# Performance work log

Measured on AMD Instinct MI355X. Metric: run time of the kernel, lower is better.

Reference implementation:

```python
import jax, jax.numpy as jnp
from jax import lax
import numpy as np

H = 64  # LSTM_HIDDEN_DIM
I = 3   # NUM_WEATHER_FEATURES


def _lstm_layer(x_seq, w_ih, w_hh, b_ih, b_hh):
    # x_seq: [B, T, in]; w_ih: [4H, in]; w_hh: [4H, H]; b_*: [4H]
    B = x_seq.shape[0]
    # Precompute input projections for all timesteps: [T, B, 4H]
    gx = jnp.einsum('bti,gi->tbg', x_seq, w_ih) + (b_ih + b_hh)
    h0 = jnp.zeros((B, H), dtype=x_seq.dtype)
    c0 = jnp.zeros((B, H), dtype=x_seq.dtype)

    def step(carry, g_t):
        h, c = carry
        gates = g_t + h @ w_hh.T  # [B, 4H]
        i, f, g, o = jnp.split(gates, 4, axis=-1)  # PyTorch gate order i,f,g,o
        i = jax.nn.sigmoid(i)
        f = jax.nn.sigmoid(f)
        g = jnp.tanh(g)
        o = jax.nn.sigmoid(o)
        c = f * c + i * g
        h = o * jnp.tanh(c)
        return (h, c), h

    (h_T, _), hs = lax.scan(step, (h0, c0), gx)
    # hs: [T, B, H] -> [B, T, H]
    return jnp.transpose(hs, (1, 0, 2)), h_T


def setup_inputs() -> dict:
    key = jax.random.key(0)
    ks = jax.random.split(key, 9)
    s = 1.0 / np.sqrt(H)  # PyTorch LSTM init scale
    x = jax.random.normal(ks[0], (4096, 365, I), dtype=jnp.float32)
    return {
        'x': x,
        'w_ih0': jax.random.uniform(ks[1], (4 * H, I), jnp.float32, -s, s),
        'w_hh0': jax.random.uniform(ks[2], (4 * H, H), jnp.float32, -s, s),
        'b_ih0': jax.random.uniform(ks[3], (4 * H,), jnp.float32, -s, s),
        'b_hh0': jax.random.uniform(ks[4], (4 * H,), jnp.float32, -s, s),
        'w_ih1': jax.random.uniform(ks[5], (4 * H, H), jnp.float32, -s, s),
        'w_hh1': jax.random.uniform(ks[6], (4 * H, H), jnp.float32, -s, s),
        'b_ih1': jax.random.uniform(ks[7], (4 * H,), jnp.float32, -s, s),
        'b_hh1': jax.random.uniform(ks[8], (4 * H,), jnp.float32, -s, s),
    }


def reference(x, w_ih0, w_hh0, b_ih0, b_hh0, w_ih1, w_hh1, b_ih1, b_hh1):
    # Layer 1 over raw features
    h1_seq, _ = _lstm_layer(x, w_ih0, w_hh0, b_ih0, b_hh0)
    # Layer 2 over layer-1 hidden states (eval mode: inter-layer dropout disabled)
    _, h2_T = _lstm_layer(h1_seq, w_ih1, w_hh1, b_ih1, b_hh1)
    # forward returns h_n[-1] == final hidden state of top layer: [B, H]
    return h2_T
```

## Files before the change

kernel.cpp:

```cpp
#include <hip/hip_runtime.h>

#define TT 365
#define NB 16
#define NTH 1024
#define XLEN (NB * TT * 3)

typedef _Float16 halfx8 __attribute__((ext_vector_type(8)));
typedef float floatx4 __attribute__((ext_vector_type(4)));
typedef float floatx2 __attribute__((ext_vector_type(2)));

#define MMH(A, B, C) __builtin_amdgcn_mfma_f32_16x16x32_f16((A), (B), (C), 0, 0, 0)

#define SGP -2.8853900817779268f
#define SGN  2.8853900817779268f
#define SS_  -1.4426950408889634f

static __device__ __forceinline__ float rcpf(float x) { return __builtin_amdgcn_rcpf(x); }
static __device__ __forceinline__ float ex2(float x)  { return __builtin_amdgcn_exp2f(x); }

#define LOADFRAG(SRC, SCALE, HI)                                               \
  do {                                                                         \
    _Pragma("unroll")                                                          \
    for (int jj = 0; jj < 8; ++jj) {                                           \
      (HI)[jj] = (_Float16)((SCALE) * (SRC)[jj]);                              \
    }                                                                          \
  } while (0)

#define PTAIL_CORE(PA, PB, CS2, HOUT)                                          \
  const floatx2 one_ = {1.0f, 1.0f};                                           \
  const floatx2 ei_ = {ex2((PA)[0]), ex2((PB)[0])};                            \
  const floatx2 ef_ = {ex2((PA)[1]), ex2((PB)[1])};                            \
  const floatx2 eg_ = {ex2((PA)[2]), ex2((PB)[2])};                            \
  const floatx2 eo_ = {ex2((PA)[3]), ex2((PB)[3])};                            \
  const floatx2 sgn2_ = {SGN, SGN};                                            \
  const floatx2 sgp2_ = {SGP, SGP};                                            \
  const floatx2 fd_ = one_ + ef_;                                              \
  const floatx2 P1_ = (one_ + ei_) * (one_ + eg_);                             \
  const floatx2 Dp_ = P1_ * fd_;                                               \
  const floatx2 R_  = {rcpf(Dp_.x), rcpf(Dp_.y)};                              \
  const floatx2 T_  = (sgn2_ * eg_ + sgp2_) * fd_;                             \
  (CS2) = ((CS2) * P1_ + T_) * R_;                                             \
  (CS2).x = fminf((CS2).x, 60.0f);                                             \
  (CS2).y = fminf((CS2).y, 60.0f);                                             \
  const floatx2 ec_ = {ex2((CS2).x), ex2((CS2).y)};                            \
  const floatx2 P2_ = (one_ + eo_) * (one_ + ec_);                             \
  const floatx2 R2_ = {rcpf(P2_.x), rcpf(P2_.y)};                              \
  const floatx2 HOUT = (one_ - ec_) * R2_;

#define PTAIL(PA, PB, CS2, ZW32, WIDX)                                         \
  do {                                                                         \
    PTAIL_CORE(PA, PB, CS2, hv_)                                               \
    (ZW32)[WIDX] =                                                             \
        __builtin_bit_cast(unsigned, __builtin_amdgcn_cvt_pkrtz(hv_.x, hv_.y)); \
  } while (0)

__global__ __launch_bounds__(NTH)
__attribute__((amdgpu_waves_per_eu(4, 4)))
void lstm2_mfma11(
    const float* __restrict__ x,
    const float* __restrict__ w_ih0, const float* __restrict__ w_hh0,
    const float* __restrict__ b_ih0, const float* __restrict__ b_hh0,
    const float* __restrict__ w_ih1, const float* __restrict__ w_hh1,
    const float* __restrict__ b_ih1, const float* __restrict__ b_hh1,
    float* __restrict__ out)
{
  __shared__ __align__(16) unsigned short Z[2][2048];
  __shared__ __align__(16) float xh[TT * 16 * 4];

  const int tid  = threadIdx.x;
  const int lane = tid & 63;
  const int wv   = tid >> 6;
  const int n15  = lane & 15;
  const int quad = lane >> 4;
  const int bbase = blockIdx.x * NB;
  const float sA = ((n15 & 3) == 2) ? SGP : SS_;

  {
    const float* xg = x + (size_t)bbase * (TT * 3);
    for (int i = tid; i < XLEN; i += NTH) {
      const int b = i / 1095;
      const int rem = i - b * 1095;
      const int t = rem / 3;
      const int c = rem - 3 * t;
      xh[(t * 16 + b) * 4 + c] = xg[i];
    }
    for (int i = tid; i < 2048; i += NTH) { Z[0][i] = 0; Z[1][i] = 0; }
  }
  unsigned short* const Zb0 = &Z[0][0];
  unsigned short* const Zb1 = &Z[1][0];
  __syncthreads();


  if (wv < 8) {
    const int w = wv;
    halfx8 a2[2][4];
    floatx4 b1v[2];
    #pragma unroll
    for (int tt = 0; tt < 2; ++tt) {
      const int arow = (n15 & 3) * 64 + 8 * w + 2 * (n15 >> 2) + tt;
      #pragma unroll
      for (int kt = 0; kt < 4; ++kt) {
        const int k0 = kt * 32 + quad * 8;
        const float* src = (k0 < 64) ? (w_ih1 + arow * 64 + k0)
                                     : (w_hh1 + arow * 64 + (k0 - 64));
        LOADFRAG(src, sA, a2[tt][kt]);
      }
      #pragma unroll
      for (int r = 0; r < 4; ++r) {
        const int crow = r * 64 + 8 * w + 2 * quad + tt;
        const float sC = (r == 2) ? SGP : SS_;
        b1v[tt][r] = sC * (b_ih1[crow] + b_hh1[crow]);
      }
    }
    const int j0 = 8 * w + 2 * quad;
    const int widx = 512 + (w >> 2) * 256 + (w & 3) * 64 + n15 * 4 + quad;
    floatx2 c2v = {0.f, 0.f};
    const halfx8* const Z0r = (const halfx8*)Zb0 + lane;
    const halfx8* const Z1r = (const halfx8*)Zb1 + lane;

    __syncthreads();

#define ESTEP(ZRP, ZW32)                                                       \
    do {                                                                       \
      const halfx8 bh0 = (ZRP)[0],   bh1 = (ZRP)[64];                          \
      const halfx8 bh2 = (ZRP)[128], bh3 = (ZRP)[192];                         \
      floatx4 e0 = b1v[0], e1 = b1v[1];                                        \
      e0 = MMH(a2[0][0], bh0, e0); e0 = MMH(a2[0][1], bh1, e0);                \
      e0 = MMH(a2[0][2], bh2, e0); e0 = MMH(a2[0][3], bh3, e0);                \
      e1 = MMH(a2[1][0], bh0, e1); e1 = MMH(a2[1][1], bh1, e1);                \
      e1 = MMH(a2[1][2], bh2, e1); e1 = MMH(a2[1][3], bh3, e1);                \
      PTAIL(e0, e1, c2v, ZW32, widx);                                          \
      __syncthreads();                                                         \
    } while (0)

    for (int it = 0; it < 182; ++it) {
      ESTEP(Z0r, (unsigned*)Zb1);
      ESTEP(Z1r, (unsigned*)Zb0);
    }

    {
      const halfx8 bh0 = Z0r[0],   bh1 = Z0r[64];
      const halfx8 bh2 = Z0r[128], bh3 = Z0r[192];
      floatx4 e0 = b1v[0], e1 = b1v[1];
      e0 = MMH(a2[0][0], bh0, e0); e0 = MMH(a2[0][1], bh1, e0);
      e0 = MMH(a2[0][2], bh2, e0); e0 = MMH(a2[0][3], bh3, e0);
      e1 = MMH(a2[1][0], bh0, e1); e1 = MMH(a2[1][1], bh1, e1);
      e1 = MMH(a2[1][2], bh2, e1); e1 = MMH(a2[1][3], bh3, e1);
      PTAIL_CORE(e0, e1, c2v, hv_)
      *(floatx2*)(out + (size_t)(bbase + n15) * 64 + j0) = hv_;
    }
  } else {
    const int u = wv - 8;
    halfx8 a1[2][2];
    floatx4 wiX[2], wiY[2], wiZ[2], b0v[2];
    #pragma unroll
    for (int tt = 0; tt < 2; ++tt) {
      const int arow = (n15 & 3) * 64 + 8 * u + 2 * (n15 >> 2) + tt;
      #pragma unroll
      for (int kt = 0; kt < 2; ++kt) {
        const float* src = w_hh0 + arow * 64 + kt * 32 + quad * 8;
        LOADFRAG(src, sA, a1[tt][kt]);
      }
      #pragma unroll
      for (int r = 0; r < 4; ++r) {
        const int crow = r * 64 + 8 * u + 2 * quad + tt;
        const float sC = (r == 2) ? SGP : SS_;
        wiX[tt][r] = sC * w_ih0[crow * 3 + 0];
        wiY[tt][r] = sC * w_ih0[crow * 3 + 1];
        wiZ[tt][r] = sC * w_ih0[crow * 3 + 2];
        b0v[tt][r] = sC * (b_ih0[crow] + b_hh0[crow]);
      }
    }
    const int widx = (u >> 2) * 256 + (u & 3) * 64 + n15 * 4 + quad;
    floatx2 c1v = {0.f, 0.f};
    const halfx8* const Z0r = (const halfx8*)Zb0 + lane;
    const halfx8* const Z1r = (const halfx8*)Zb1 + lane;

    {
      const floatx4 xv = *(const floatx4*)(xh + n15 * 4);
      const floatx4 s0 = {xv[0], xv[0], xv[0], xv[0]};
      const floatx4 s1 = {xv[1], xv[1], xv[1], xv[1]};
      const floatx4 s2 = {xv[2], xv[2], xv[2], xv[2]};
      floatx4 d0 = __builtin_elementwise_fma(wiX[0], s0,
                     __builtin_elementwise_fma(wiY[0], s1,
                       __builtin_elementwise_fma(wiZ[0], s2, b0v[0])));
      floatx4 d1 = __builtin_elementwise_fma(wiX[1], s0,
                     __builtin_elementwise_fma(wiY[1], s1,
                       __builtin_elementwise_fma(wiZ[1], s2, b0v[1])));
      PTAIL(d0, d1, c1v, (unsigned*)Zb0, widx);
    }
    __syncthreads();

    const float* xp = xh + 64 + n15 * 4;

#define DSTEP(ZRP, ZW32)                                                       \
    do {                                                                       \
      const halfx8 bh0 = (ZRP)[0], bh1 = (ZRP)[64];                            \
      const floatx4 xv = *(const floatx4*)xp;                                  \
      const floatx4 s0 = {xv[0], xv[0], xv[0], xv[0]};                         \
      const floatx4 s1 = {xv[1], xv[1], xv[1], xv[1]};                         \
      const floatx4 s2 = {xv[2], xv[2], xv[2], xv[2]};                         \
      floatx4 d0 = __builtin_elementwise_fma(wiX[0], s0,                       \
                     __builtin_elementwise_fma(wiY[0], s1,                     \
                       __builtin_elementwise_fma(wiZ[0], s2, b0v[0])));        \
      floatx4 d1 = __builtin_elementwise_fma(wiX[1], s0,                       \
                     __builtin_elementwise_fma(wiY[1], s1,                     \
                       __builtin_elementwise_fma(wiZ[1], s2, b0v[1])));        \
      d0 = MMH(a1[0][0], bh0, d0); d0 = MMH(a1[0][1], bh1, d0);                \
      d1 = MMH(a1[1][0], bh0, d1); d1 = MMH(a1[1][1], bh1, d1);                \
      PTAIL(d0, d1, c1v, ZW32, widx);                                          \
      xp += 64;                                                                \
      __syncthreads();                                                         \
    } while (0)

    for (int it = 0; it < 182; ++it) {
      DSTEP(Z0r, (unsigned*)Zb1);
      DSTEP(Z1r, (unsigned*)Zb0);
    }
  }
}

extern "C" void kernel_launch(void* const* d_in, const int* in_sizes, int n_in,
                              void* d_out, int out_size, void* d_ws, size_t ws_size,
                              hipStream_t stream) {
  const float* x     = (const float*)d_in[0];
  const float* w_ih0 = (const float*)d_in[1];
  const float* w_hh0 = (const float*)d_in[2];
  const float* b_ih0 = (const float*)d_in[3];
  const float* b_hh0 = (const float*)d_in[4];
  const float* w_ih1 = (const float*)d_in[5];
  const float* w_hh1 = (const float*)d_in[6];
  const float* b_ih1 = (const float*)d_in[7];
  const float* b_hh1 = (const float*)d_in[8];
  float* out = (float*)d_out;

  const int B = in_sizes[0] / (TT * 3);
  const int grid = B / NB;

  lstm2_mfma11<<<dim3(grid), dim3(NTH), 0, stream>>>(
      x, w_ih0, w_hh0, b_ih0, b_hh0, w_ih1, w_hh1, b_ih1, b_hh1, out);
}
```

Measured before the change: 304.1 us.

## Replace block-wide barriers with LDS counter flags between layer warp groups

Replaces the per-timestep __syncthreads shared by both LSTM layers with per-group atomic counters in LDS and spin-waits, so layer-1 waves can run up to three steps ahead of layer-2 waves. Layer-1 hidden states move to a four-slot ring buffer and layer-2 states to a separate double buffer. The aim is to decouple the two layers' critical paths and remove full-block barrier stalls. In exchange, every wave spins on LDS atomic loads, which adds LDS traffic and instruction-issue contention, and correctness relies on the fences and release/acquire ordering.

```diff
diff --git a/kernel.cpp b/kernel.cpp
--- a/kernel.cpp
+++ b/kernel.cpp
@@ -17,6 +17,15 @@
 
 static __device__ __forceinline__ float rcpf(float x) { return __builtin_amdgcn_rcpf(x); }
 static __device__ __forceinline__ float ex2(float x)  { return __builtin_amdgcn_exp2f(x); }
+
+static __device__ __forceinline__ void publish(unsigned* c, int lane) {
+  __threadfence_block();
+  if (lane == 0)
+    __hip_atomic_fetch_add(c, 1u, __ATOMIC_RELEASE, __HIP_MEMORY_SCOPE_WORKGROUP);
+}
+static __device__ __forceinline__ void spin_ge(unsigned* c, unsigned tgt) {
+  while (__hip_atomic_load(c, __ATOMIC_ACQUIRE, __HIP_MEMORY_SCOPE_WORKGROUP) < tgt) { }
+}
 
 #define LOADFRAG(SRC, SCALE, HI)                                               \
   do {                                                                         \
@@ -56,7 +65,7 @@
 
 __global__ __launch_bounds__(NTH)
 __attribute__((amdgpu_waves_per_eu(4, 4)))
-void lstm2_mfma11(
+void lstm2_mfma17(
     const float* __restrict__ x,
     const float* __restrict__ w_ih0, const float* __restrict__ w_hh0,
     const float* __restrict__ b_ih0, const float* __restrict__ b_hh0,
@@ -64,8 +73,10 @@
     const float* __restrict__ b_ih1, const float* __restrict__ b_hh1,
     float* __restrict__ out)
 {
-  __shared__ __align__(16) unsigned short Z[2][2048];
+  __shared__ __align__(16) unsigned short Zh1[4][1024];
+  __shared__ __align__(16) unsigned short Zh2[2][1024];
   __shared__ __align__(16) float xh[TT * 16 * 4];
+  __shared__ unsigned cnt[16];
 
   const int tid  = threadIdx.x;
   const int lane = tid & 63;
@@ -84,12 +95,11 @@
       const int c = rem - 3 * t;
       xh[(t * 16 + b) * 4 + c] = xg[i];
     }
-    for (int i = tid; i < 2048; i += NTH) { Z[0][i] = 0; Z[1][i] = 0; }
+    for (int i = tid; i < 4096; i += NTH) (&Zh1[0][0])[i] = 0;
+    for (int i = tid; i < 2048; i += NTH) (&Zh2[0][0])[i] = 0;
+    if (tid < 16) cnt[tid] = 0;
   }
-  unsigned short* const Zb0 = &Z[0][0];
-  unsigned short* const Zb1 = &Z[1][0];
   __syncthreads();
-
 
   if (wv < 8) {
     const int w = wv;
@@ -113,34 +123,34 @@
       }
     }
     const int j0 = 8 * w + 2 * quad;
-    const int widx = 512 + (w >> 2) * 256 + (w & 3) * 64 + n15 * 4 + quad;
+    const int widx = (w >> 2) * 256 + (w & 3) * 64 + n15 * 4 + quad;
     floatx2 c2v = {0.f, 0.f};
-    const halfx8* const Z0r = (const halfx8*)Zb0 + lane;
-    const halfx8* const Z1r = (const halfx8*)Zb1 + lane;
-
-    __syncthreads();
-
-#define ESTEP(ZRP, ZW32)                                                       \
-    do {                                                                       \
-      const halfx8 bh0 = (ZRP)[0],   bh1 = (ZRP)[64];                          \
-      const halfx8 bh2 = (ZRP)[128], bh3 = (ZRP)[192];                         \
-      floatx4 e0 = b1v[0], e1 = b1v[1];                                        \
-      e0 = MMH(a2[0][0], bh0, e0); e0 = MMH(a2[0][1], bh1, e0);                \
-      e0 = MMH(a2[0][2], bh2, e0); e0 = MMH(a2[0][3], bh3, e0);                \
-      e1 = MMH(a2[1][0], bh0, e1); e1 = MMH(a2[1][1], bh1, e1);                \
-      e1 = MMH(a2[1][2], bh2, e1); e1 = MMH(a2[1][3], bh3, e1);                \
-      PTAIL(e0, e1, c2v, ZW32, widx);                                          \
-      __syncthreads();                                                         \
-    } while (0)
-
-    for (int it = 0; it < 182; ++it) {
-      ESTEP(Z0r, (unsigned*)Zb1);
-      ESTEP(Z1r, (unsigned*)Zb0);
+
+    #pragma unroll 4
+    for (int t = 0; t < 364; ++t) {
+      spin_ge(&cnt[8], 8u * (unsigned)t);
+      spin_ge(&cnt[0], 8u * (unsigned)(t + 1));
+      const halfx8* r1 = (const halfx8*)(&Zh1[t & 3][0]) + lane;
+      const halfx8* r2 = (const halfx8*)(&Zh2[t & 1][0]) + lane;
+      const halfx8 bh0 = r1[0], bh1 = r1[64];
+      const halfx8 bh2 = r2[0], bh3 = r2[64];
+      floatx4 e0 = b1v[0], e1 = b1v[1];
+      e0 = MMH(a2[0][0], bh0, e0); e0 = MMH(a2[0][1], bh1, e0);
+      e0 = MMH(a2[0][2], bh2, e0); e0 = MMH(a2[0][3], bh3, e0);
+      e1 = MMH(a2[1][0], bh0, e1); e1 = MMH(a2[1][1], bh1, e1);
+      e1 = MMH(a2[1][2], bh2, e1); e1 = MMH(a2[1][3], bh3, e1);
+      unsigned* zw = (unsigned*)(&Zh2[(t + 1) & 1][0]);
+      PTAIL(e0, e1, c2v, zw, widx);
+      publish(&cnt[8], lane);
     }
 
     {
-      const halfx8 bh0 = Z0r[0],   bh1 = Z0r[64];
-      const halfx8 bh2 = Z0r[128], bh3 = Z0r[192];
+      spin_ge(&cnt[8], 8u * 364u);
+      spin_ge(&cnt[0], 8u * 365u);
+      const halfx8* r1 = (const halfx8*)(&Zh1[364 & 3][0]) + lane;
+      const halfx8* r2 = (const halfx8*)(&Zh2[364 & 1][0]) + lane;
+      const halfx8 bh0 = r1[0], bh1 = r1[64];
+      const halfx8 bh2 = r2[0], bh3 = r2[64];
       floatx4 e0 = b1v[0], e1 = b1v[1];
       e0 = MMH(a2[0][0], bh0, e0); e0 = MMH(a2[0][1], bh1, e0);
       e0 = MMH(a2[0][2], bh2, e0); e0 = MMH(a2[0][3], bh3, e0);
@@ -173,8 +183,6 @@
     }
     const int widx = (u >> 2) * 256 + (u & 3) * 64 + n15 * 4 + quad;
     floatx2 c1v = {0.f, 0.f};
-    const halfx8* const Z0r = (const halfx8*)Zb0 + lane;
-    const halfx8* const Z1r = (const halfx8*)Zb1 + lane;
 
     {
       const floatx4 xv = *(const floatx4*)(xh + n15 * 4);
@@ -187,35 +195,31 @@
       floatx4 d1 = __builtin_elementwise_fma(wiX[1], s0,
                      __builtin_elementwise_fma(wiY[1], s1,
                        __builtin_elementwise_fma(wiZ[1], s2, b0v[1])));
-      PTAIL(d0, d1, c1v, (unsigned*)Zb0, widx);
-    }
-    __syncthreads();
-
-    const float* xp = xh + 64 + n15 * 4;
-
-#define DSTEP(ZRP, ZW32)                                                       \
-    do {                                                                       \
-      const halfx8 bh0 = (ZRP)[0], bh1 = (ZRP)[64];                            \
-      const floatx4 xv = *(const floatx4*)xp;                                  \
-      const floatx4 s0 = {xv[0], xv[0], xv[0], xv[0]};                         \
-      const floatx4 s1 = {xv[1], xv[1], xv[1], xv[1]};                         \
-      const floatx4 s2 = {xv[2], xv[2], xv[2], xv[2]};                         \
-      floatx4 d0 = __builtin_elementwise_fma(wiX[0], s0,                       \
-                     __builtin_elementwise_fma(wiY[0], s1,                     \
-                       __builtin_elementwise_fma(wiZ[0], s2, b0v[0])));        \
-      floatx4 d1 = __builtin_elementwise_fma(wiX[1], s0,                       \
-                     __builtin_elementwise_fma(wiY[1], s1,                     \
-                       __builtin_elementwise_fma(wiZ[1], s2, b0v[1])));        \
-      d0 = MMH(a1[0][0], bh0, d0); d0 = MMH(a1[0][1], bh1, d0);                \
-      d1 = MMH(a1[1][0], bh0, d1); d1 = MMH(a1[1][1], bh1, d1);                \
-      PTAIL(d0, d1, c1v, ZW32, widx);                                          \
-      xp += 64;                                                                \
-      __syncthreads();                                                         \
-    } while (0)
-
-    for (int it = 0; it < 182; ++it) {
-      DSTEP(Z0r, (unsigned*)Zb1);
-      DSTEP(Z1r, (unsigned*)Zb0);
+      PTAIL(d0, d1, c1v, (unsigned*)(&Zh1[0][0]), widx);
+      publish(&cnt[0], lane);
+    }
+
+    #pragma unroll 4
+    for (int t = 1; t < 365; ++t) {
+      spin_ge(&cnt[0], 8u * (unsigned)t);
+      if (t >= 4) spin_ge(&cnt[8], 8u * (unsigned)(t - 3));
+      const halfx8* rp = (const halfx8*)(&Zh1[(t - 1) & 3][0]) + lane;
+      const halfx8 bh0 = rp[0], bh1 = rp[64];
+      const floatx4 xv = *(const floatx4*)(xh + t * 64 + n15 * 4);
+      const floatx4 s0 = {xv[0], xv[0], xv[0], xv[0]};
+      const floatx4 s1 = {xv[1], xv[1], xv[1], xv[1]};
+      const floatx4 s2 = {xv[2], xv[2], xv[2], xv[2]};
+      floatx4 d0 = __builtin_elementwise_fma(wiX[0], s0,
+                     __builtin_elementwise_fma(wiY[0], s1,
+                       __builtin_elementwise_fma(wiZ[0], s2, b0v[0])));
+      floatx4 d1 = __builtin_elementwise_fma(wiX[1], s0,
+                     __builtin_elementwise_fma(wiY[1], s1,
+                       __builtin_elementwise_fma(wiZ[1], s2, b0v[1])));
+      d0 = MMH(a1[0][0], bh0, d0); d0 = MMH(a1[0][1], bh1, d0);
+      d1 = MMH(a1[1][0], bh0, d1); d1 = MMH(a1[1][1], bh1, d1);
+      unsigned* zw = (unsigned*)(&Zh1[t & 3][0]);
+      PTAIL(d0, d1, c1v, zw, widx);
+      publish(&cnt[0], lane);
     }
   }
 }
@@ -237,6 +241,6 @@
   const int B = in_sizes[0] / (TT * 3);
   const int grid = B / NB;
 
-  lstm2_mfma11<<<dim3(grid), dim3(NTH), 0, stream>>>(
+  lstm2_mfma17<<<dim3(grid), dim3(NTH), 0, stream>>>(
       x, w_ih0, w_hh0, b_ih0, b_hh0, w_ih1, w_hh1, b_ih1, b_hh1, out);
 }
```

Result: slower. 345.1 us (+13.5%).

## Give every wave one layer-1 and one layer-2 hidden unit instead of splitting waves by layer

Applied to the files above, without the earlier changes.

Before, waves 0-7 ran layer 2 and waves 8-15 ran layer 1, each handling two hidden rows. Now all 16 waves handle one row of both layers, so layer-1 and layer-2 gate math is packed into the same floatx2 tail and the per-wave work is balanced. The intent is to remove the imbalance where layer-1 waves (fewer MFMAs) idle at the barrier, and to use the two-lane tail for both layers at once. The shared-memory write layout changes to 16-bit scattered stores, which may add LDS bank conflicts.

```diff
diff --git a/kernel.cpp b/kernel.cpp
--- a/kernel.cpp
+++ b/kernel.cpp
@@ -47,16 +47,9 @@
   const floatx2 R2_ = {rcpf(P2_.x), rcpf(P2_.y)};                              \
   const floatx2 HOUT = (one_ - ec_) * R2_;
 
-#define PTAIL(PA, PB, CS2, ZW32, WIDX)                                         \
-  do {                                                                         \
-    PTAIL_CORE(PA, PB, CS2, hv_)                                               \
-    (ZW32)[WIDX] =                                                             \
-        __builtin_bit_cast(unsigned, __builtin_amdgcn_cvt_pkrtz(hv_.x, hv_.y)); \
-  } while (0)
-
 __global__ __launch_bounds__(NTH)
 __attribute__((amdgpu_waves_per_eu(4, 4)))
-void lstm2_mfma11(
+void lstm2_mfma19(
     const float* __restrict__ x,
     const float* __restrict__ w_ih0, const float* __restrict__ w_hh0,
     const float* __restrict__ b_ih0, const float* __restrict__ b_hh0,
@@ -72,6 +65,8 @@
   const int wv   = tid >> 6;
   const int n15  = lane & 15;
   const int quad = lane >> 4;
+  const int wu   = wv & 7;
+  const int ttw  = wv >> 3;
   const int bbase = blockIdx.x * NB;
   const float sA = ((n15 & 3) == 2) ? SGP : SS_;
 
@@ -86,137 +81,97 @@
     }
     for (int i = tid; i < 2048; i += NTH) { Z[0][i] = 0; Z[1][i] = 0; }
   }
-  unsigned short* const Zb0 = &Z[0][0];
-  unsigned short* const Zb1 = &Z[1][0];
   __syncthreads();
 
+  halfx8 a1[2], a2[4];
+  floatx4 wiX, wiY, wiZ, b0v, b1v;
+  {
+    const int arow = (n15 & 3) * 64 + 8 * wu + 2 * (n15 >> 2) + ttw;
+    #pragma unroll
+    for (int kt = 0; kt < 4; ++kt) {
+      const int k0 = kt * 32 + quad * 8;
+      const float* src = (k0 < 64) ? (w_ih1 + arow * 64 + k0)
+                                   : (w_hh1 + arow * 64 + (k0 - 64));
+      LOADFRAG(src, sA, a2[kt]);
+    }
+    #pragma unroll
+    for (int kt = 0; kt < 2; ++kt) {
+      const float* src = w_hh0 + arow * 64 + kt * 32 + quad * 8;
+      LOADFRAG(src, sA, a1[kt]);
+    }
+  }
+  const int u = 8 * wu + 2 * quad + ttw;
+  #pragma unroll
+  for (int r = 0; r < 4; ++r) {
+    const int crow = r * 64 + u;
+    const float sC = (r == 2) ? SGP : SS_;
+    wiX[r] = sC * w_ih0[crow * 3 + 0];
+    wiY[r] = sC * w_ih0[crow * 3 + 1];
+    wiZ[r] = sC * w_ih0[crow * 3 + 2];
+    b0v[r] = sC * (b_ih0[crow] + b_hh0[crow]);
+    b1v[r] = sC * (b_ih1[crow] + b_hh1[crow]);
+  }
+  const int widx1 = (u >> 5) * 512 + (((u >> 3) & 3) * 16 + n15) * 8 + (u & 7);
+  const int widx2 = widx1 + 1024;
+  floatx2 cs = {0.f, 0.f};
 
-  if (wv < 8) {
-    const int w = wv;
-    halfx8 a2[2][4];
-    floatx4 b1v[2];
-    #pragma unroll
-    for (int tt = 0; tt < 2; ++tt) {
-      const int arow = (n15 & 3) * 64 + 8 * w + 2 * (n15 >> 2) + tt;
-      #pragma unroll
-      for (int kt = 0; kt < 4; ++kt) {
-        const int k0 = kt * 32 + quad * 8;
-        const float* src = (k0 < 64) ? (w_ih1 + arow * 64 + k0)
-                                     : (w_hh1 + arow * 64 + (k0 - 64));
-        LOADFRAG(src, sA, a2[tt][kt]);
-      }
-      #pragma unroll
-      for (int r = 0; r < 4; ++r) {
-        const int crow = r * 64 + 8 * w + 2 * quad + tt;
-        const float sC = (r == 2) ? SGP : SS_;
-        b1v[tt][r] = sC * (b_ih1[crow] + b_hh1[crow]);
-      }
-    }
-    const int j0 = 8 * w + 2 * quad;
-    const int widx = 512 + (w >> 2) * 256 + (w & 3) * 64 + n15 * 4 + quad;
-    floatx2 c2v = {0.f, 0.f};
-    const halfx8* const Z0r = (const halfx8*)Zb0 + lane;
-    const halfx8* const Z1r = (const halfx8*)Zb1 + lane;
+  unsigned short* const Zs0 = &Z[0][0];
+  unsigned short* const Zs1 = &Z[1][0];
+  const halfx8* const Z0r = (const halfx8*)Zs0 + lane;
+  const halfx8* const Z1r = (const halfx8*)Zs1 + lane;
 
-    __syncthreads();
+  {
+    const floatx4 xv = *(const floatx4*)(xh + n15 * 4);
+    const floatx4 s0 = {xv[0], xv[0], xv[0], xv[0]};
+    const floatx4 s1 = {xv[1], xv[1], xv[1], xv[1]};
+    const floatx4 s2 = {xv[2], xv[2], xv[2], xv[2]};
+    floatx4 d0 = __builtin_elementwise_fma(wiX, s0,
+                   __builtin_elementwise_fma(wiY, s1,
+                     __builtin_elementwise_fma(wiZ, s2, b0v)));
+    PTAIL_CORE(d0, d0, cs, hv_)
+    const unsigned pk =
+        __builtin_bit_cast(unsigned, __builtin_amdgcn_cvt_pkrtz(hv_.x, hv_.x));
+    Zs0[widx1] = (unsigned short)pk;
+    cs.y = 0.f;
+  }
+  __syncthreads();
 
-#define ESTEP(ZRP, ZW32)                                                       \
-    do {                                                                       \
-      const halfx8 bh0 = (ZRP)[0],   bh1 = (ZRP)[64];                          \
-      const halfx8 bh2 = (ZRP)[128], bh3 = (ZRP)[192];                         \
-      floatx4 e0 = b1v[0], e1 = b1v[1];                                        \
-      e0 = MMH(a2[0][0], bh0, e0); e0 = MMH(a2[0][1], bh1, e0);                \
-      e0 = MMH(a2[0][2], bh2, e0); e0 = MMH(a2[0][3], bh3, e0);                \
-      e1 = MMH(a2[1][0], bh0, e1); e1 = MMH(a2[1][1], bh1, e1);                \
-      e1 = MMH(a2[1][2], bh2, e1); e1 = MMH(a2[1][3], bh3, e1);                \
-      PTAIL(e0, e1, c2v, ZW32, widx);                                          \
-      __syncthreads();                                                         \
-    } while (0)
+#define STEP(ZRP, ZW, XT)                                                      \
+  do {                                                                         \
+    const halfx8 bh0 = (ZRP)[0],   bh1 = (ZRP)[64];                            \
+    const halfx8 bh2 = (ZRP)[128], bh3 = (ZRP)[192];                           \
+    const floatx4 xv = *(const floatx4*)(xh + (XT) * 64 + n15 * 4);            \
+    const floatx4 s0 = {xv[0], xv[0], xv[0], xv[0]};                           \
+    const floatx4 s1 = {xv[1], xv[1], xv[1], xv[1]};                           \
+    const floatx4 s2 = {xv[2], xv[2], xv[2], xv[2]};                           \
+    floatx4 d0 = __builtin_elementwise_fma(wiX, s0,                            \
+                   __builtin_elementwise_fma(wiY, s1,                          \
+                     __builtin_elementwise_fma(wiZ, s2, b0v)));                \
+    floatx4 e0 = b1v;                                                          \
+    e0 = MMH(a2[0], bh0, e0); e0 = MMH(a2[1], bh1, e0);                        \
+    e0 = MMH(a2[2], bh2, e0); e0 = MMH(a2[3], bh3, e0);                        \
+    d0 = MMH(a1[0], bh0, d0); d0 = MMH(a1[1], bh1, d0);                        \
+    PTAIL_CORE(d0, e0, cs, hv_)                                                \
+    const unsigned pk =                                                        \
+        __builtin_bit_cast(unsigned, __builtin_amdgcn_cvt_pkrtz(hv_.x, hv_.y)); \
+    (ZW)[widx1] = (unsigned short)pk;                                          \
+    (ZW)[widx2] = (unsigned short)(pk >> 16);                                  \
+    __syncthreads();                                                           \
+  } while (0)
 
-    for (int it = 0; it < 182; ++it) {
-      ESTEP(Z0r, (unsigned*)Zb1);
-      ESTEP(Z1r, (unsigned*)Zb0);
-    }
+  for (int p = 0; p < 364; p += 2) {
+    STEP(Z0r, Zs1, p + 1);
+    STEP(Z1r, Zs0, p + 2);
+  }
 
-    {
-      const halfx8 bh0 = Z0r[0],   bh1 = Z0r[64];
-      const halfx8 bh2 = Z0r[128], bh3 = Z0r[192];
-      floatx4 e0 = b1v[0], e1 = b1v[1];
-      e0 = MMH(a2[0][0], bh0, e0); e0 = MMH(a2[0][1], bh1, e0);
-      e0 = MMH(a2[0][2], bh2, e0); e0 = MMH(a2[0][3], bh3, e0);
-      e1 = MMH(a2[1][0], bh0, e1); e1 = MMH(a2[1][1], bh1, e1);
-      e1 = MMH(a2[1][2], bh2, e1); e1 = MMH(a2[1][3], bh3, e1);
-      PTAIL_CORE(e0, e1, c2v, hv_)
-      *(floatx2*)(out + (size_t)(bbase + n15) * 64 + j0) = hv_;
-    }
-  } else {
-    const int u = wv - 8;
-    halfx8 a1[2][2];
-    floatx4 wiX[2], wiY[2], wiZ[2], b0v[2];
-    #pragma unroll
-    for (int tt = 0; tt < 2; ++tt) {
-      const int arow = (n15 & 3) * 64 + 8 * u + 2 * (n15 >> 2) + tt;
-      #pragma unroll
-      for (int kt = 0; kt < 2; ++kt) {
-        const float* src = w_hh0 + arow * 64 + kt * 32 + quad * 8;
-        LOADFRAG(src, sA, a1[tt][kt]);
-      }
-      #pragma unroll
-      for (int r = 0; r < 4; ++r) {
-        const int crow = r * 64 + 8 * u + 2 * quad + tt;
-        const float sC = (r == 2) ? SGP : SS_;
-        wiX[tt][r] = sC * w_ih0[crow * 3 + 0];
-        wiY[tt][r] = sC * w_ih0[crow * 3 + 1];
-        wiZ[tt][r] = sC * w_ih0[crow * 3 + 2];
-        b0v[tt][r] = sC * (b_ih0[crow] + b_hh0[crow]);
-      }
-    }
-    const int widx = (u >> 2) * 256 + (u & 3) * 64 + n15 * 4 + quad;
-    floatx2 c1v = {0.f, 0.f};
-    const halfx8* const Z0r = (const halfx8*)Zb0 + lane;
-    const halfx8* const Z1r = (const halfx8*)Zb1 + lane;
-
-    {
-      const floatx4 xv = *(const floatx4*)(xh + n15 * 4);
-      const floatx4 s0 = {xv[0], xv[0], xv[0], xv[0]};
-      const floatx4 s1 = {xv[1], xv[1], xv[1], xv[1]};
-      const floatx4 s2 = {xv[2], xv[2], xv[2], xv[2]};
-      floatx4 d0 = __builtin_elementwise_fma(wiX[0], s0,
-                     __builtin_elementwise_fma(wiY[0], s1,
-                       __builtin_elementwise_fma(wiZ[0], s2, b0v[0])));
-      floatx4 d1 = __builtin_elementwise_fma(wiX[1], s0,
-                     __builtin_elementwise_fma(wiY[1], s1,
-                       __builtin_elementwise_fma(wiZ[1], s2, b0v[1])));
-      PTAIL(d0, d1, c1v, (unsigned*)Zb0, widx);
-    }
-    __syncthreads();
-
-    const float* xp = xh + 64 + n15 * 4;
-
-#define DSTEP(ZRP, ZW32)                                                       \
-    do {                                                                       \
-      const halfx8 bh0 = (ZRP)[0], bh1 = (ZRP)[64];                            \
-      const floatx4 xv = *(const floatx4*)xp;                                  \
-      const floatx4 s0 = {xv[0], xv[0], xv[0], xv[0]};                         \
-      const floatx4 s1 = {xv[1], xv[1], xv[1], xv[1]};                         \
-      const floatx4 s2 = {xv[2], xv[2], xv[2], xv[2]};                         \
-      floatx4 d0 = __builtin_elementwise_fma(wiX[0], s0,                       \
-                     __builtin_elementwise_fma(wiY[0], s1,                     \
-                       __builtin_elementwise_fma(wiZ[0], s2, b0v[0])));        \
-      floatx4 d1 = __builtin_elementwise_fma(wiX[1], s0,                       \
-                     __builtin_elementwise_fma(wiY[1], s1,                     \
-                       __builtin_elementwise_fma(wiZ[1], s2, b0v[1])));        \
-      d0 = MMH(a1[0][0], bh0, d0); d0 = MMH(a1[0][1], bh1, d0);                \
-      d1 = MMH(a1[1][0], bh0, d1); d1 = MMH(a1[1][1], bh1, d1);                \
-      PTAIL(d0, d1, c1v, ZW32, widx);                                          \
-      xp += 64;                                                                \
-      __syncthreads();                                                         \
-    } while (0)
-
-    for (int it = 0; it < 182; ++it) {
-      DSTEP(Z0r, (unsigned*)Zb1);
-      DSTEP(Z1r, (unsigned*)Zb0);
-    }
+  {
+    const halfx8 bh0 = Z0r[0],   bh1 = Z0r[64];
+    const halfx8 bh2 = Z0r[128], bh3 = Z0r[192];
+    floatx4 e0 = b1v;
+    e0 = MMH(a2[0], bh0, e0); e0 = MMH(a2[1], bh1, e0);
+    e0 = MMH(a2[2], bh2, e0); e0 = MMH(a2[3], bh3, e0);
+    PTAIL_CORE(e0, e0, cs, hv_)
+    out[(size_t)(bbase + n15) * 64 + u] = hv_.y;
   }
 }
 
@@ -237,6 +192,6 @@
   const int B = in_sizes[0] / (TT * 3);
   const int grid = B / NB;
 
-  lstm2_mfma11<<<dim3(grid), dim3(NTH), 0, stream>>>(
+  lstm2_mfma19<<<dim3(grid), dim3(NTH), 0, stream>>>(
       x, w_ih0, w_hh0, b_ih0, b_hh0, w_ih1, w_hh1, b_ih1, b_hh1, out);
 }
```

After: 330.4 us. 1.09x slower.
